# Optimization experiments

Measured on AMD Instinct MI355X. Metric: run time of the kernel, lower is better.

The kernel has to match this reference:

```python
import jax, jax.numpy as jnp
import numpy as np

# Model dims (match init_kwargs)
B, L, C = 4, 4096, 1024   # batch, seq_len, dim
M = 128                   # memory_dim
P = 4                     # n_persistent
S = 64                    # segment_size
H = 8                     # num_heads in nn.MultiheadAttention


def _ln(x, g, b, eps=1e-5):
    mu = jnp.mean(x, -1, keepdims=True)
    var = jnp.mean((x - mu) ** 2, -1, keepdims=True)
    return (x - mu) * jax.lax.rsqrt(var + eps) * g + b


def setup_inputs() -> dict:
    key = jax.random.key(0)
    ks = jax.random.split(key, 16)
    def n(k, shape, s=0.02):
        return jax.random.normal(k, shape, jnp.float32) * s
    return {
        "x": jax.random.normal(ks[0], (B, L, C), jnp.float32),
        "persistent_memory": n(ks[1], (1, P, C)),
        "Wq": n(ks[2], (C, C)),            # query_proj (no bias)
        "Wk": n(ks[3], (C, C)),            # key_proj (no bias)
        "Wv": n(ks[4], (C, C)),            # value_proj (no bias)
        # NeuralMemoryModule.memory_net: Linear(C->M), SiLU, LN(M), Linear(M->M), LN(M)
        "mem_W1": n(ks[5], (M, C)), "mem_b1": jnp.zeros((M,)),
        "mem_ln1_g": jnp.ones((M,)), "mem_ln1_b": jnp.zeros((M,)),
        "mem_W2": n(ks[6], (M, M)), "mem_b2": jnp.zeros((M,)),
        "mem_ln2_g": jnp.ones((M,)), "mem_ln2_b": jnp.zeros((M,)),
        "mem_out_W": n(ks[7], (C, M)), "mem_out_b": jnp.zeros((C,)),
        "memory_state": jnp.zeros((1, M)),  # persistent buffer (zeros at init)
        # nn.MultiheadAttention in/out projections
        "mha_Wq": n(ks[8], (C, C)), "mha_bq": jnp.zeros((C,)),
        "mha_Wk": n(ks[9], (C, C)), "mha_bk": jnp.zeros((C,)),
        "mha_Wv": n(ks[10], (C, C)), "mha_bv": jnp.zeros((C,)),
        "mha_Wo": n(ks[11], (C, C)), "mha_bo": jnp.zeros((C,)),
        "gn_g": jnp.ones((C,)), "gn_b": jnp.zeros((C,)),   # gate_norm
        "gate_W": n(ks[12], (C, C)), "gate_b": jnp.zeros((C,)),
        "out_W": n(ks[13], (C, C)), "out_b": jnp.zeros((C,)),
    }


def reference(x, persistent_memory, Wq, Wk, Wv,
              mem_W1, mem_b1, mem_ln1_g, mem_ln1_b,
              mem_W2, mem_b2, mem_ln2_g, mem_ln2_b,
              mem_out_W, mem_out_b, memory_state,
              mha_Wq, mha_bq, mha_Wk, mha_bk, mha_Wv, mha_bv, mha_Wo, mha_bo,
              gn_g, gn_b, gate_W, gate_b, out_W, out_b):
    Bx, Lx, Cx = x.shape
    n_seg = Lx // S
    # Eval-mode: memory_state is frozen, so all segments are independent ->
    # process every segment in parallel instead of a Python loop over L.
    xs = x.reshape(Bx * n_seg, S, Cx)           # [N, S, C]
    q_seg = xs @ Wq.T                            # query_proj
    # retrieve from long-term memory: memory_net(queries) + memory_state -> output_proj
    h = jax.nn.silu(q_seg @ mem_W1.T + mem_b1)
    h = _ln(h, mem_ln1_g, mem_ln1_b)
    h = h @ mem_W2.T + mem_b2
    h = _ln(h, mem_ln2_g, mem_ln2_b)             # [N, S, M]
    retrieved = (h + memory_state[0]) @ mem_out_W.T + mem_out_b  # [N, S, C]
    # context = [retrieved_memory, persistent_memory, current_segment]
    pm = jnp.broadcast_to(persistent_memory, (Bx * n_seg, P, Cx))
    context = jnp.concatenate([retrieved, pm, xs], axis=1)       # [N, T, C], T=S+P+S
    k_in = context @ Wk.T
    v_in = context @ Wv.T
    T = context.shape[1]
    hd = Cx // H
    q = (q_seg @ mha_Wq.T + mha_bq).reshape(-1, S, H, hd)
    k = (k_in @ mha_Wk.T + mha_bk).reshape(-1, T, H, hd)
    v = (v_in @ mha_Wv.T + mha_bv).reshape(-1, T, H, hd)
    scores = jnp.einsum('nshd,nthd->nhst', q, k) / jnp.sqrt(jnp.float32(hd))
    attn = jnp.einsum('nhst,nthd->nshd', jax.nn.softmax(scores, -1), v)
    attn = attn.reshape(-1, S, Cx) @ mha_Wo.T + mha_bo           # [N, S, C]
    # learned gate blend + output projection
    gate = jax.nn.sigmoid(_ln(attn, gn_g, gn_b) @ gate_W.T + gate_b)
    out = (gate * attn + xs) @ out_W.T + out_b
    return out.reshape(Bx, Lx, Cx)
```

## Files before the change

### kernel.cpp

```cpp
#include <hip/hip_runtime.h>
#include <hip/hip_bf16.h>
#include <math.h>


using bf16 = __hip_bfloat16;

typedef __attribute__((ext_vector_type(8))) short bf16x8;
typedef __attribute__((ext_vector_type(4))) float f32x4;

__device__ __forceinline__ float ldf(const bf16* p) { return __bfloat162float(*p); }
__device__ __forceinline__ float ldf(const float* p) { return *p; }
__device__ __forceinline__ void stf(bf16* p, float v) { *p = __float2bfloat16(v); }
__device__ __forceinline__ void stf(float* p, float v) { *p = v; }
__device__ __forceinline__ float b2f(const bf16& b) { return __bfloat162float(b); }
__device__ __forceinline__ float bsf(short s) {
  union { unsigned u; float f; } cv;
  cv.u = (unsigned)(unsigned short)s << 16;
  return cv.f;
}

enum { ACT_NONE = 0, ACT_SILU = 1, ACT_SIGMOID = 2, ACT_GATE = 3, ACT_PSILU = 4 };

__global__ void detect_kernel(const unsigned short* g, int* flag) {
  if (threadIdx.x == 0) *flag = (g[0] != 0) ? 1 : 0;
}

struct ConvArgs {
  const void* src[29];
  bf16* dst[29];
  int n[29];
  int bstart[30];
};

__global__ __launch_bounds__(256) void convall_kernel(ConvArgs a, const int* __restrict__ flag) {
  int b = blockIdx.x;
  int ti = 0;
  while (ti < 28 && b >= a.bstart[ti + 1]) ++ti;
  int i = (b - a.bstart[ti]) * 256 + threadIdx.x;
  if (i >= a.n[ti]) return;
  if (*flag) a.dst[ti][i] = ((const bf16*)a.src[ti])[i];
  else a.dst[ti][i] = __float2bfloat16(((const float*)a.src[ti])[i]);
}

__global__ __launch_bounds__(256) void conv_kernel(
    const void* __restrict__ src, bf16* __restrict__ dst, int n, size_t src_off,
    const int* __restrict__ flag) {
  int i = blockIdx.x * 256 + threadIdx.x;
  if (i >= n) return;
  if (*flag) dst[i] = ((const bf16*)src)[src_off + i];
  else dst[i] = __float2bfloat16(((const float*)src)[src_off + i]);
}

__global__ __launch_bounds__(256) void pack_bias4(
    const bf16* __restrict__ bk, const bf16* __restrict__ bv,
    const bf16* __restrict__ bq, const bf16* __restrict__ b1,
    bf16* __restrict__ o) {
  int j = blockIdx.x * 256 + threadIdx.x;
  if (j >= 3200) return;
  float v;
  if (j < 1024) v = b2f(bk[j]);
  else if (j < 2048) v = b2f(bv[j - 1024]);
  else if (j < 3072) v = b2f(bq[j - 2048]);
  else v = b2f(b1[j - 3072]);
  o[j] = __float2bfloat16(v);
}

__global__ __launch_bounds__(256) void transpose_kernel(
    const bf16* __restrict__ srcb, bf16* __restrict__ dstb, int rows, int cols) {
  __shared__ unsigned short t[64][72];
  const unsigned short* src = (const unsigned short*)srcb;
  unsigned short* dst = (unsigned short*)dstb;
  const int r0 = blockIdx.y * 64, c0 = blockIdx.x * 64;
  for (int e = threadIdx.x; e < 64 * 8; e += 256) {
    int r = e >> 3, c8 = e & 7;
    uint4 v = *(const uint4*)(src + (size_t)(r0 + r) * cols + c0 + c8 * 8);
    *(uint4*)&t[r][c8 * 8] = v;
  }
  __syncthreads();
  for (int e = threadIdx.x; e < 64 * 8; e += 256) {
    int c = e >> 3, r8 = (e & 7) * 8;
    unsigned short v[8];
#pragma unroll
    for (int j = 0; j < 8; ++j) v[j] = t[r8 + j][c];
    *(uint4*)(dst + (size_t)(c0 + c) * rows + r0 + r8) = *(uint4*)v;
  }
}

__global__ __launch_bounds__(256) void kpvp_kernel(
    const bf16* __restrict__ pmb, const bf16* __restrict__ mobb,
    const bf16* __restrict__ Wb, const bf16* __restrict__ bias4b,
    bf16* __restrict__ kp, bf16* __restrict__ vp, bf16* __restrict__ bkv)
{
  const short* pm = (const short*)pmb;
  const short* mob = (const short*)mobb;
  const short* W = (const short*)Wb;
  const int wave = threadIdx.x >> 6, lane = threadIdx.x & 63;
  const int c = blockIdx.x * 4 + wave;
  const short* wrow = W + (size_t)c * 1024 + lane * 16;
  const bf16x8 w0 = *(const bf16x8*)wrow;
  const bf16x8 w1 = *(const bf16x8*)(wrow + 8);
  float acc[5];
#pragma unroll
  for (int m = 0; m < 5; ++m) {
    const short* prow = (m < 4) ? (pm + m * 1024 + lane * 16) : (mob + lane * 16);
    const bf16x8 p0 = *(const bf16x8*)prow;
    const bf16x8 p1 = *(const bf16x8*)(prow + 8);
    float s = 0.f;
#pragma unroll
    for (int j = 0; j < 8; ++j) s += bsf(w0[j]) * bsf(p0[j]) + bsf(w1[j]) * bsf(p1[j]);
    acc[m] = s;
  }
#pragma unroll
  for (int d = 1; d < 64; d <<= 1) {
#pragma unroll
    for (int m = 0; m < 5; ++m) acc[m] += __shfl_xor(acc[m], d);
  }
  if (lane == 0) {
    const float bv = b2f(bias4b[c]);
    bf16* dst = (c < 1024) ? (kp + c) : (vp + (c - 1024));
#pragma unroll
    for (int m = 0; m < 4; ++m) stf(dst + m * 1024, acc[m] + bv);
    stf(&bkv[c], acc[4] + bv);
  }
}

__device__ __forceinline__ void gl_lds16(const short* g, short* l) {
  __builtin_amdgcn_global_load_lds(
      (const __attribute__((address_space(1))) void*)g,
      (__attribute__((address_space(3))) void*)l, 16, 0, 0);
}

template <typename TC, int ACT, bool HAS_BIAS>
__global__ __launch_bounds__(256) void mgemm(
    const bf16* __restrict__ Ab, const bf16* __restrict__ Bw,
    const bf16* __restrict__ bias, TC* __restrict__ C,
    int M, int N, int K, int lda, int ldc,
    const bf16* __restrict__ ao, const void* __restrict__ xsrc, size_t xoff,
    const int* __restrict__ flag, int pn)
{
  __shared__ short As[128 * 32];
  __shared__ short Bs[128 * 32];
  const short* A = (const short*)Ab;
  const short* B = (const short*)Bw;
  const int tid = threadIdx.x;
  const int m0 = blockIdx.x * 128, n0 = blockIdx.y * 128;
  const int wave = tid >> 6, lane = tid & 63;
  const int wm = (wave & 1) * 64, wn = (wave >> 1) * 64;
  const int fm = lane & 15;
  const int fk = (lane >> 4) * 8;

  const int srow = tid >> 2, scol = (tid & 3) * 8;
  const short* gA0 = A + (size_t)(m0 + srow) * lda + scol;
  const short* gA1 = A + (size_t)(m0 + 64 + srow) * lda + scol;
  const short* gB0 = B + (size_t)(n0 + srow) * K + scol;
  const short* gB1 = B + (size_t)(n0 + 64 + srow) * K + scol;
  short* lA0 = As + tid * 8;
  short* lA1 = As + (256 + tid) * 8;
  short* lB0 = Bs + tid * 8;
  short* lB1 = Bs + (256 + tid) * 8;

  f32x4 acc[4][4] = {};

  for (int k0 = 0; k0 < K; k0 += 32) {
    gl_lds16(gA0 + k0, lA0);
    gl_lds16(gA1 + k0, lA1);
    gl_lds16(gB0 + k0, lB0);
    gl_lds16(gB1 + k0, lB1);
    __syncthreads();
    bf16x8 af[4], bfr[4];
#pragma unroll
    for (int i = 0; i < 4; ++i)
      af[i] = *(const bf16x8*)&As[(wm + i * 16 + fm) * 32 + fk];
#pragma unroll
    for (int j = 0; j < 4; ++j)
      bfr[j] = *(const bf16x8*)&Bs[(wn + j * 16 + fm) * 32 + fk];
#pragma unroll
    for (int i = 0; i < 4; ++i)
#pragma unroll
      for (int j = 0; j < 4; ++j)
        acc[i][j] = __builtin_amdgcn_mfma_f32_16x16x32_bf16(af[i], bfr[j], acc[i][j], 0, 0, 0);
    __syncthreads();
  }

  const int rg = (lane >> 4) * 4;
#pragma unroll
  for (int i = 0; i < 4; ++i) {
#pragma unroll
    for (int j = 0; j < 4; ++j) {
      const int n = n0 + wn + j * 16 + fm;
      float bv = 0.f;
      if (HAS_BIAS) bv = b2f(bias[n]);
#pragma unroll
      for (int r = 0; r < 4; ++r) {
        const int m = m0 + wm + i * 16 + rg + r;
        float v = acc[i][j][r] + bv;
        if (ACT == ACT_SILU) v = v / (1.f + __expf(-v));
        if (ACT == ACT_PSILU) { if (n >= pn) v = v / (1.f + __expf(-v)); }
        if (ACT == ACT_SIGMOID) v = 1.f / (1.f + __expf(-v));
        if (ACT == ACT_GATE) {
          v = 1.f / (1.f + __expf(-v));
          const size_t e = (size_t)m * 1024 + n;
          const float xv = *flag ? b2f(((const bf16*)xsrc)[xoff + e])
                                 : ((const float*)xsrc)[xoff + e];
          v = v * b2f(ao[e]) + xv;
        }
        stf(&C[(size_t)m * ldc + n], v);
      }
    }
  }
}

__global__ __launch_bounds__(256) void kgemm(
    const bf16* __restrict__ Ab, const bf16* __restrict__ Bw,
    float* __restrict__ P, int M, int N, int K, int lda)
{
  __shared__ short As[128 * 32];
  __shared__ short Bs[128 * 32];
  const short* A = (const short*)Ab;
  const short* B = (const short*)Bw;
  const int tid = threadIdx.x;
  const int m0 = blockIdx.x * 128, n0 = blockIdx.y * 128;
  const int kb = blockIdx.z * (K >> 2), ke = kb + (K >> 2);
  const int wave = tid >> 6, lane = tid & 63;
  const int wm = (wave & 1) * 64, wn = (wave >> 1) * 64;
  const int fm = lane & 15;
  const int fk = (lane >> 4) * 8;

  const int srow = tid >> 2, scol = (tid & 3) * 8;
  const short* gA0 = A + (size_t)(m0 + srow) * lda + scol;
  const short* gA1 = A + (size_t)(m0 + 64 + srow) * lda + scol;
  const short* gB0 = B + (size_t)(n0 + srow) * K + scol;
  const short* gB1 = B + (size_t)(n0 + 64 + srow) * K + scol;
  short* lA0 = As + tid * 8;
  short* lA1 = As + (256 + tid) * 8;
  short* lB0 = Bs + tid * 8;
  short* lB1 = Bs + (256 + tid) * 8;

  f32x4 acc[4][4] = {};

  for (int k0 = kb; k0 < ke; k0 += 32) {
    gl_lds16(gA0 + k0, lA0);
    gl_lds16(gA1 + k0, lA1);
    gl_lds16(gB0 + k0, lB0);
    gl_lds16(gB1 + k0, lB1);
    __syncthreads();
    bf16x8 af[4], bfr[4];
#pragma unroll
    for (int i = 0; i < 4; ++i)
      af[i] = *(const bf16x8*)&As[(wm + i * 16 + fm) * 32 + fk];
#pragma unroll
    for (int j = 0; j < 4; ++j)
      bfr[j] = *(const bf16x8*)&Bs[(wn + j * 16 + fm) * 32 + fk];
#pragma unroll
    for (int i = 0; i < 4; ++i)
#pragma unroll
      for (int j = 0; j < 4; ++j)
        acc[i][j] = __builtin_amdgcn_mfma_f32_16x16x32_bf16(af[i], bfr[j], acc[i][j], 0, 0, 0);
    __syncthreads();
  }

  float* Cp = P + (size_t)blockIdx.z * ((size_t)M * N);
  const int rg = (lane >> 4) * 4;
#pragma unroll
  for (int i = 0; i < 4; ++i)
#pragma unroll
    for (int j = 0; j < 4; ++j) {
      const int n = n0 + wn + j * 16 + fm;
#pragma unroll
      for (int r = 0; r < 4; ++r) {
        const int m = m0 + wm + i * 16 + rg + r;
        Cp[(size_t)m * N + n] = acc[i][j][r];
      }
    }
}

__global__ __launch_bounds__(256) void foldfin_kernel(
    const float* __restrict__ P, bf16* __restrict__ o, int MN) {
  int i = blockIdx.x * 256 + threadIdx.x;
  if (i >= MN) return;
  float s = P[i] + P[i + (size_t)MN] + P[i + 2 * (size_t)MN] + P[i + 3 * (size_t)MN];
  o[i] = __float2bfloat16(s);
}

template <typename TI, typename TO, bool ADD, int W, int BS>
__global__ __launch_bounds__(BS) void ln_kernel(
    const TI* __restrict__ in, const bf16* __restrict__ g, const bf16* __restrict__ b,
    const bf16* __restrict__ addv, TO* __restrict__ out, int ldin)
{
  __shared__ float red[BS];
  const int row = blockIdx.x;
  const TI* rin = in + (size_t)row * ldin;
  TO* rout = out + (size_t)row * W;
  const int NP = W / BS;
  float v[NP];
  float s = 0.f;
#pragma unroll
  for (int i = 0; i < NP; ++i) { v[i] = ldf(&rin[threadIdx.x + i * BS]); s += v[i]; }
  red[threadIdx.x] = s; __syncthreads();
  for (int o = BS / 2; o > 0; o >>= 1) {
    if (threadIdx.x < o) red[threadIdx.x] += red[threadIdx.x + o];
    __syncthreads();
  }
  const float mean = red[0] / W;
  __syncthreads();
  float sq = 0.f;
#pragma unroll
  for (int i = 0; i < NP; ++i) { float d = v[i] - mean; sq += d * d; }
  red[threadIdx.x] = sq; __syncthreads();
  for (int o = BS / 2; o > 0; o >>= 1) {
    if (threadIdx.x < o) red[threadIdx.x] += red[threadIdx.x + o];
    __syncthreads();
  }
  const float rstd = rsqrtf(red[0] / W + 1e-5f);
#pragma unroll
  for (int i = 0; i < NP; ++i) {
    int c = threadIdx.x + i * BS;
    float o_ = (v[i] - mean) * rstd * b2f(g[c]) + b2f(b[c]);
    if (ADD) o_ += b2f(addv[c]);
    stf(&rout[c], o_);
  }
}

__global__ __launch_bounds__(512) void attn_kernel(
    const bf16* __restrict__ qg, int str_q,
    const bf16* __restrict__ krv, int str_r,
    const bf16* __restrict__ kxv, int str_x, const bf16* __restrict__ kpg,
    const bf16* __restrict__ vpg, bf16* __restrict__ outg)
{
  __shared__ short qs[4 * 64 * 32];
  __shared__ short ksl[4 * 144 * 32];
  __shared__ short vt[128 * 168];
  __shared__ short pl[64 * 168];

  const int tid = threadIdx.x;
  unsigned bid = blockIdx.x;
  {
    const unsigned nwg = gridDim.x;
    const unsigned q_ = nwg >> 3, r_ = nwg & 7;
    const unsigned xcd = bid & 7, loc = bid >> 3;
    bid = (xcd < r_ ? xcd * (q_ + 1) : r_ * (q_ + 1) + (xcd - r_) * q_) + loc;
  }
  const int seg = (int)(bid >> 3), h = (int)(bid & 7);
  const unsigned short* q = (const unsigned short*)qg + (size_t)seg * 64 * str_q + h * 128;
  const unsigned short* kv_r = (const unsigned short*)krv + (size_t)seg * 64 * str_r + h * 128;
  const unsigned short* kv_x = (const unsigned short*)kxv + (size_t)seg * 64 * str_x + h * 128;
  const unsigned short* kp = (const unsigned short*)kpg;
  const unsigned short* vp = (const unsigned short*)vpg;
  const size_t obase = (size_t)seg * 64 * 1024 + h * 128;

  for (int ch = tid; ch < 64 * 16; ch += 512) {
    int row = ch >> 4, k8 = ch & 15;
    uint4 v = *(const uint4*)(q + (size_t)row * str_q + k8 * 8);
    *(uint4*)&qs[((k8 >> 2) * 64 + row) * 32 + (k8 & 3) * 8] = v;
  }
  for (int ch = tid; ch < 132 * 16; ch += 512) {
    int t = ch >> 4, k8 = ch & 15;
    const unsigned short* src;
    if (t < 64) src = kv_r + (size_t)t * str_r;
    else if (t < 68) src = kp + (size_t)(t - 64) * 1024 + h * 128;
    else src = kv_x + (size_t)(t - 68) * str_x;
    uint4 v = *(const uint4*)(src + k8 * 8);
    *(uint4*)&ksl[((k8 >> 2) * 144 + t) * 32 + (k8 & 3) * 8] = v;
  }
  __syncthreads();

  const int wave = tid >> 6, lane = tid & 63;
  const int fm = lane & 15, fq = lane >> 4;

  if (wave < 4) {
    const int s0 = wave * 16;
    f32x4 acc[10];
#pragma unroll
    for (int tt = 0; tt < 10; ++tt) acc[tt] = (f32x4){0.f, 0.f, 0.f, 0.f};
#pragma unroll
    for (int kb = 0; kb < 4; ++kb) {
      const bf16x8 a = *(const bf16x8*)&qs[(kb * 64 + s0 + fm) * 32 + fq * 8];
#pragma unroll
      for (int tt = 0; tt < 9; ++tt) {
        const bf16x8 b = *(const bf16x8*)&ksl[(kb * 144 + tt * 16 + fm) * 32 + fq * 8];
        acc[tt] = __builtin_amdgcn_mfma_f32_16x16x32_bf16(a, b, acc[tt], 0, 0, 0);
      }
    }
    const float scale = 0.08838834764831845f;
#pragma unroll
    for (int r = 0; r < 4; ++r) {
      float m = -3.0e38f;
#pragma unroll
      for (int tt = 0; tt < 9; ++tt) {
        int t = tt * 16 + fm;
        if (t < 132) m = fmaxf(m, acc[tt][r] * scale);
      }
      for (int d = 1; d < 16; d <<= 1) m = fmaxf(m, __shfl_xor(m, d));
      float e[10];
      float sum = 0.f;
#pragma unroll
      for (int tt = 0; tt < 10; ++tt) {
        int t = tt * 16 + fm;
        float ev = 0.f;
        if (t < 132) ev = __expf(acc[tt][r] * scale - m);
        e[tt] = ev; sum += ev;
      }
      for (int d = 1; d < 16; d <<= 1) sum += __shfl_xor(sum, d);
      const float inv = 1.f / sum;
      const int s = s0 + fq * 4 + r;
#pragma unroll
      for (int tt = 0; tt < 10; ++tt) {
        bf16 pv = __float2bfloat16(e[tt] * inv);
        pl[s * 168 + tt * 16 + fm] = *(const short*)&pv;
      }
    }
  } else {
    for (int ch = tid - 256; ch < 132 * 32; ch += 256) {
      int t = ch >> 5, d4 = (ch & 31) * 4;
      const unsigned short* src;
      if (t < 64) src = kv_r + 1024 + (size_t)t * str_r;
      else if (t < 68) src = vp + (size_t)(t - 64) * 1024 + h * 128;
      else src = kv_x + 1024 + (size_t)(t - 68) * str_x;
      uint2 w = *(const uint2*)(src + d4);
      vt[(d4 + 0) * 168 + t] = (short)(w.x & 0xffffu);
      vt[(d4 + 1) * 168 + t] = (short)(w.x >> 16);
      vt[(d4 + 2) * 168 + t] = (short)(w.y & 0xffffu);
      vt[(d4 + 3) * 168 + t] = (short)(w.y >> 16);
    }
    for (int ch = tid - 256; ch < 128 * 32; ch += 256) {
      int d = ch >> 5, tp = 132 + (ch & 31);
      vt[d * 168 + tp] = 0;
    }
  }
  __syncthreads();

  const int dt = wave;
  bf16x8 af[5];
#pragma unroll
  for (int kb = 0; kb < 5; ++kb)
    af[kb] = *(const bf16x8*)&vt[(dt * 16 + fm) * 168 + kb * 32 + fq * 8];
#pragma unroll
  for (int st = 0; st < 4; ++st) {
    f32x4 o = (f32x4){0.f, 0.f, 0.f, 0.f};
#pragma unroll
    for (int kb = 0; kb < 5; ++kb) {
      const bf16x8 bp = *(const bf16x8*)&pl[(st * 16 + fm) * 168 + kb * 32 + fq * 8];
      o = __builtin_amdgcn_mfma_f32_16x16x32_bf16(af[kb], bp, o, 0, 0, 0);
    }
    const int s = st * 16 + fm;
    bf16 b0 = __float2bfloat16(o[0]), b1 = __float2bfloat16(o[1]);
    bf16 b2 = __float2bfloat16(o[2]), b3 = __float2bfloat16(o[3]);
    uint2 w;
    w.x = ((unsigned)(*(unsigned short*)&b1) << 16) | (*(unsigned short*)&b0);
    w.y = ((unsigned)(*(unsigned short*)&b3) << 16) | (*(unsigned short*)&b2);
    *(uint2*)((unsigned short*)outg + obase + (size_t)s * 1024 + dt * 16 + fq * 4) = w;
  }
}

extern "C" void kernel_launch(void* const* d_in, const int* in_sizes, int n_in,
                              void* d_out, int out_size, void* d_ws, size_t ws_size,
                              hipStream_t stream)
{
  (void)n_in; (void)out_size;
  const int R = 16384, Cd = 1024;

  char* ws = (char*)d_ws;
  size_t off = 0;
  auto alloc = [&](size_t bytes) -> void* {
    void* p = ws + off;
    off += (bytes + 255) & ~(size_t)255;
    return p;
  };

  int* flag = (int*)alloc(256);
  bf16* W4    = (bf16*)alloc((size_t)3200 * Cd * sizeof(bf16));
  bf16* bias4 = (bf16*)alloc(3200 * sizeof(bf16));
  bf16* T     = (bf16*)alloc((size_t)Cd * Cd * sizeof(bf16));
  bf16* Wc    = (bf16*)alloc((size_t)2048 * 128 * sizeof(bf16));
  bf16* kp    = (bf16*)alloc((size_t)4 * Cd * sizeof(bf16));
  bf16* vp    = (bf16*)alloc((size_t)4 * Cd * sizeof(bf16));
  bf16* bkv   = (bf16*)alloc(2048 * sizeof(bf16));
  bf16* WqStk = (bf16*)alloc((size_t)1152 * Cd * sizeof(bf16));
  bf16* nb[30];
  nb[0] = nullptr;
  for (int i = 1; i < 30; ++i) nb[i] = (bf16*)alloc((size_t)in_sizes[i] * sizeof(bf16));
  nb[16] = WqStk;
  nb[5]  = WqStk + (size_t)1024 * Cd;
  const size_t fixed_end = off;

  size_t avail = (ws_size > fixed_end + (1u << 20)) ? (ws_size - fixed_end - (1u << 20)) : 0;
  int crmax = (int)(avail / 17152);
  if (crmax > R) crmax = R;
  if (crmax < 128) crmax = 128;
  int nch = (R + crmax - 1) / crmax;
  int CR = ((R / nch + 127) / 128) * 128;
  while (CR * nch < R) CR += 128;

  const size_t chunk_start = off;
  const size_t RB = (size_t)CR * Cd * sizeof(bf16);
  bf16* Xc  = (bf16*)alloc(RB);
  bf16* QS4 = (bf16*)alloc((size_t)CR * 3200 * sizeof(bf16));
  bf16* h1b = (bf16*)alloc((size_t)CR * 128 * sizeof(bf16));
  bf16* h2b = (bf16*)alloc((size_t)CR * 128 * sizeof(bf16));
  bf16* Bb  = (bf16*)alloc(RB);
  bf16* KVr = (bf16*)alloc(2 * RB);
  bf16* Cc  = (bf16*)alloc(RB);
  const size_t chunk_bytes = off - chunk_start;

  dim3 blk(256);
  auto g128 = [](int M_, int N_) { return dim3((unsigned)(M_ / 128), (unsigned)(N_ / 128)); };

  detect_kernel<<<1, 64, 0, stream>>>((const unsigned short*)d_in[24], flag);
  {
    ConvArgs a;
    int bs = 0;
    for (int i = 1; i < 30; ++i) {
      a.src[i - 1] = d_in[i];
      a.dst[i - 1] = nb[i];
      a.n[i - 1] = in_sizes[i];
      a.bstart[i - 1] = bs;
      bs += (in_sizes[i] + 255) / 256;
    }
    a.bstart[29] = bs;
    convall_kernel<<<dim3((unsigned)bs), blk, 0, stream>>>(a, flag);
  }
  const bf16 *pm = nb[1], *Wq = nb[2], *Wk = nb[3], *Wv = nb[4];
  const bf16 *mem_W1 = nb[5], *mem_b1 = nb[6], *ln1g = nb[7], *ln1b = nb[8];
  const bf16 *mem_W2 = nb[9], *mem_b2 = nb[10], *ln2g = nb[11], *ln2b = nb[12];
  const bf16 *mem_oW = nb[13], *mem_ob = nb[14], *mstate = nb[15];
  const bf16 *mhaWq = nb[16], *mhabq = nb[17], *mhaWk = nb[18], *mhabk = nb[19];
  const bf16 *mhaWv = nb[20], *mhabv = nb[21], *mhaWo = nb[22], *mhabo = nb[23];
  const bf16 *gn_g = nb[24], *gn_b = nb[25], *gateW = nb[26], *gateb = nb[27];
  const bf16 *outW = nb[28], *outb = nb[29];
  bf16* Wkk = W4;
  bf16* Wvv = W4 + (size_t)1024 * Cd;
  bf16* Wqq = W4 + (size_t)2048 * Cd;
  bf16* Wm1 = W4 + (size_t)3072 * Cd;

  const bool use_ks = chunk_bytes >= (size_t)4 * 1152 * 1024 * sizeof(float);
  if (use_ks) {
    float* P = (float*)Xc;
    transpose_kernel<<<dim3(16, 16), blk, 0, stream>>>(Wq, T, 1024, 1024);
    kgemm<<<dim3(9, 8, 4), blk, 0, stream>>>(WqStk, T, P, 1152, 1024, 1024, 1024);
    foldfin_kernel<<<dim3(4608), blk, 0, stream>>>(P, Wqq, 1152 * 1024);
    transpose_kernel<<<dim3(16, 16), blk, 0, stream>>>(Wk, T, 1024, 1024);
    kgemm<<<dim3(8, 8, 4), blk, 0, stream>>>(mhaWk, T, P, 1024, 1024, 1024, 1024);
    foldfin_kernel<<<dim3(4096), blk, 0, stream>>>(P, Wkk, 1024 * 1024);
    transpose_kernel<<<dim3(16, 16), blk, 0, stream>>>(Wv, T, 1024, 1024);
    kgemm<<<dim3(8, 8, 4), blk, 0, stream>>>(mhaWv, T, P, 1024, 1024, 1024, 1024);
    foldfin_kernel<<<dim3(4096), blk, 0, stream>>>(P, Wvv, 1024 * 1024);
    transpose_kernel<<<dim3(2, 16), blk, 0, stream>>>(mem_oW, T, 1024, 128);
    kgemm<<<dim3(16, 1, 4), blk, 0, stream>>>(W4, T, P, 2048, 128, 1024, 1024);
    foldfin_kernel<<<dim3(1024), blk, 0, stream>>>(P, Wc, 2048 * 128);
  } else {
    transpose_kernel<<<dim3(16, 16), blk, 0, stream>>>(Wq, T, 1024, 1024);
    mgemm<bf16, ACT_NONE, false><<<g128(1024, 1024), blk, 0, stream>>>(
        mhaWq, T, nullptr, Wqq, 1024, 1024, 1024, 1024, 1024, nullptr, nullptr, 0, nullptr, 0);
    mgemm<bf16, ACT_NONE, false><<<g128(128, 1024), blk, 0, stream>>>(
        mem_W1, T, nullptr, Wm1, 128, 1024, 1024, 1024, 1024, nullptr, nullptr, 0, nullptr, 0);
    transpose_kernel<<<dim3(16, 16), blk, 0, stream>>>(Wk, T, 1024, 1024);
    mgemm<bf16, ACT_NONE, false><<<g128(1024, 1024), blk, 0, stream>>>(
        mhaWk, T, nullptr, Wkk, 1024, 1024, 1024, 1024, 1024, nullptr, nullptr, 0, nullptr, 0);
    transpose_kernel<<<dim3(16, 16), blk, 0, stream>>>(Wv, T, 1024, 1024);
    mgemm<bf16, ACT_NONE, false><<<g128(1024, 1024), blk, 0, stream>>>(
        mhaWv, T, nullptr, Wvv, 1024, 1024, 1024, 1024, 1024, nullptr, nullptr, 0, nullptr, 0);
    transpose_kernel<<<dim3(2, 16), blk, 0, stream>>>(mem_oW, T, 1024, 128);
    mgemm<bf16, ACT_NONE, false><<<g128(2048, 128), blk, 0, stream>>>(
        W4, T, nullptr, Wc, 2048, 128, 1024, 1024, 128, nullptr, nullptr, 0, nullptr, 0);
  }
  pack_bias4<<<13, blk, 0, stream>>>(mhabk, mhabv, mhabq, mem_b1, bias4);
  kpvp_kernel<<<dim3(512), blk, 0, stream>>>(pm, mem_ob, W4, bias4, kp, vp, bkv);

  for (int r0 = 0; r0 < R; r0 += CR) {
    const int cr = (R - r0 < CR) ? (R - r0) : CR;
    const int n = cr * Cd;
    conv_kernel<<<dim3((n + 255) / 256), blk, 0, stream>>>(d_in[0], Xc, n, (size_t)r0 * Cd, flag);

    mgemm<bf16, ACT_PSILU, true><<<g128(cr, 3200), blk, 0, stream>>>(
        Xc, W4, bias4, QS4, cr, 3200, 1024, 1024, 3200, nullptr, nullptr, 0, nullptr, 3072);

    ln_kernel<bf16, bf16, false, 128, 128><<<cr, 128, 0, stream>>>(
        QS4 + 3072, ln1g, ln1b, nullptr, h2b, 3200);
    mgemm<bf16, ACT_NONE, true><<<g128(cr, 128), blk, 0, stream>>>(
        h2b, mem_W2, mem_b2, h1b, cr, 128, 128, 128, 128, nullptr, nullptr, 0, nullptr, 0);
    ln_kernel<bf16, bf16, true, 128, 128><<<cr, 128, 0, stream>>>(h1b, ln2g, ln2b, mstate, h2b, 128);
    mgemm<bf16, ACT_NONE, true><<<g128(cr, 2048), blk, 0, stream>>>(
        h2b, Wc, bkv, KVr, cr, 2048, 128, 128, 2048, nullptr, nullptr, 0, nullptr, 0);

    attn_kernel<<<dim3((cr / 64) * 8), dim3(512), 0, stream>>>(
        QS4 + 2048, 3200, KVr, 2048, QS4, 3200, kp, vp, Xc);

    mgemm<bf16, ACT_NONE, true><<<g128(cr, Cd), blk, 0, stream>>>(
        Xc, mhaWo, mhabo, Bb, cr, Cd, Cd, Cd, Cd, nullptr, nullptr, 0, nullptr, 0);
    ln_kernel<bf16, bf16, false, 1024, 256><<<cr, 256, 0, stream>>>(Bb, gn_g, gn_b, nullptr, Cc, Cd);
    mgemm<bf16, ACT_GATE, true><<<g128(cr, Cd), blk, 0, stream>>>(
        Cc, gateW, gateb, Xc, cr, Cd, Cd, Cd, Cd, Bb, d_in[0], (size_t)r0 * Cd, flag, 0);
    mgemm<float, ACT_NONE, true><<<g128(cr, Cd), blk, 0, stream>>>(
        Xc, outW, outb, (float*)d_out + (size_t)r0 * Cd, cr, Cd, Cd, Cd, Cd,
        nullptr, nullptr, 0, nullptr, 0);
  }
}
```

Baseline: 884.1 us.

## Double-buffer GEMM LDS tiles with XOR swizzle and vectorize input conversion

The mgemm main loop now keeps two LDS buffers and issues the global-to-LDS loads for tile k+2 while tile k is being multiplied. Raw s_waitcnt and s_barrier calls replace the full __syncthreads pairs, so load latency can overlap with MFMA work. An XOR swizzle on the k-chunk index is applied both when writing LDS and when reading fragments, to reduce bank conflicts. The conv kernel now handles 8 elements per thread with 16-byte loads and stores. The costs are twice the LDS per block, which may lower occupancy, and the loop assumes K is at least 64 and n is a multiple of 8.

```diff
diff --git a/kernel.cpp b/kernel.cpp
--- a/kernel.cpp
+++ b/kernel.cpp
@@ -45,10 +45,21 @@
 __global__ __launch_bounds__(256) void conv_kernel(
     const void* __restrict__ src, bf16* __restrict__ dst, int n, size_t src_off,
     const int* __restrict__ flag) {
-  int i = blockIdx.x * 256 + threadIdx.x;
+  int i = (blockIdx.x * 256 + threadIdx.x) * 8;
   if (i >= n) return;
-  if (*flag) dst[i] = ((const bf16*)src)[src_off + i];
-  else dst[i] = __float2bfloat16(((const float*)src)[src_off + i]);
+  if (*flag) {
+    *(uint4*)((unsigned short*)dst + i) =
+        *(const uint4*)((const unsigned short*)src + src_off + i);
+  } else {
+    const float* s = (const float*)src + src_off + i;
+    const float4 a = *(const float4*)s;
+    const float4 b = *(const float4*)(s + 4);
+    bf16 t[8] = {__float2bfloat16(a.x), __float2bfloat16(a.y),
+                 __float2bfloat16(a.z), __float2bfloat16(a.w),
+                 __float2bfloat16(b.x), __float2bfloat16(b.y),
+                 __float2bfloat16(b.z), __float2bfloat16(b.w)};
+    *(uint4*)((unsigned short*)dst + i) = *(const uint4*)t;
+  }
 }
 
 __global__ __launch_bounds__(256) void pack_bias4(
@@ -138,8 +149,8 @@
     const bf16* __restrict__ ao, const void* __restrict__ xsrc, size_t xoff,
     const int* __restrict__ flag, int pn)
 {
-  __shared__ short As[128 * 32];
-  __shared__ short Bs[128 * 32];
+  __shared__ short As[2][128 * 32];
+  __shared__ short Bs[2][128 * 32];
   const short* A = (const short*)Ab;
   const short* B = (const short*)Bw;
   const int tid = threadIdx.x;
@@ -147,42 +158,54 @@
   const int wave = tid >> 6, lane = tid & 63;
   const int wm = (wave & 1) * 64, wn = (wave >> 1) * 64;
   const int fm = lane & 15;
-  const int fk = (lane >> 4) * 8;
-
-  const int srow = tid >> 2, scol = (tid & 3) * 8;
+  const int fq = lane >> 4;
+  const int fks = (fq ^ ((fm >> 1) & 3)) * 8;
+
+  const int srow = tid >> 2;
+  const int scol = ((tid & 3) ^ ((tid >> 3) & 3)) * 8;
   const short* gA0 = A + (size_t)(m0 + srow) * lda + scol;
   const short* gA1 = A + (size_t)(m0 + 64 + srow) * lda + scol;
   const short* gB0 = B + (size_t)(n0 + srow) * K + scol;
   const short* gB1 = B + (size_t)(n0 + 64 + srow) * K + scol;
-  short* lA0 = As + tid * 8;
-  short* lA1 = As + (256 + tid) * 8;
-  short* lB0 = Bs + tid * 8;
-  short* lB1 = Bs + (256 + tid) * 8;
 
   f32x4 acc[4][4] = {};
-
-  for (int k0 = 0; k0 < K; k0 += 32) {
-    gl_lds16(gA0 + k0, lA0);
-    gl_lds16(gA1 + k0, lA1);
-    gl_lds16(gB0 + k0, lB0);
-    gl_lds16(gB1 + k0, lB1);
-    __syncthreads();
+  const int NT = K >> 5;
+
+#define STAGE(buf, k0)                              \
+  do {                                              \
+    gl_lds16(gA0 + (k0), &As[buf][tid * 8]);        \
+    gl_lds16(gA1 + (k0), &As[buf][(256 + tid) * 8]);\
+    gl_lds16(gB0 + (k0), &Bs[buf][tid * 8]);        \
+    gl_lds16(gB1 + (k0), &Bs[buf][(256 + tid) * 8]);\
+  } while (0)
+
+  STAGE(0, 0);
+  STAGE(1, 32);
+
+  for (int kt = 0; kt < NT; ++kt) {
+    const int cur = kt & 1;
+    if (kt == NT - 1) asm volatile("s_waitcnt vmcnt(0)" ::: "memory");
+    else              asm volatile("s_waitcnt vmcnt(4)" ::: "memory");
+    __builtin_amdgcn_s_barrier();
     bf16x8 af[4], bfr[4];
 #pragma unroll
     for (int i = 0; i < 4; ++i)
-      af[i] = *(const bf16x8*)&As[(wm + i * 16 + fm) * 32 + fk];
+      af[i] = *(const bf16x8*)&As[cur][(wm + i * 16 + fm) * 32 + fks];
 #pragma unroll
     for (int j = 0; j < 4; ++j)
-      bfr[j] = *(const bf16x8*)&Bs[(wn + j * 16 + fm) * 32 + fk];
+      bfr[j] = *(const bf16x8*)&Bs[cur][(wn + j * 16 + fm) * 32 + fks];
 #pragma unroll
     for (int i = 0; i < 4; ++i)
 #pragma unroll
       for (int j = 0; j < 4; ++j)
         acc[i][j] = __builtin_amdgcn_mfma_f32_16x16x32_bf16(af[i], bfr[j], acc[i][j], 0, 0, 0);
-    __syncthreads();
-  }
-
-  const int rg = (lane >> 4) * 4;
+    asm volatile("s_waitcnt lgkmcnt(0)" ::: "memory");
+    __builtin_amdgcn_s_barrier();
+    if (kt + 2 < NT) STAGE(cur, (kt + 2) * 32);
+  }
+#undef STAGE
+
+  const int rg = fq * 4;
 #pragma unroll
   for (int i = 0; i < 4; ++i) {
 #pragma unroll
@@ -569,7 +592,8 @@
   for (int r0 = 0; r0 < R; r0 += CR) {
     const int cr = (R - r0 < CR) ? (R - r0) : CR;
     const int n = cr * Cd;
-    conv_kernel<<<dim3((n + 255) / 256), blk, 0, stream>>>(d_in[0], Xc, n, (size_t)r0 * Cd, flag);
+    conv_kernel<<<dim3((n / 8 + 255) / 256), blk, 0, stream>>>(
+        d_in[0], Xc, n, (size_t)r0 * Cd, flag);
 
     mgemm<bf16, ACT_PSILU, true><<<g128(cr, 3200), blk, 0, stream>>>(
         Xc, W4, bias4, QS4, cr, 3200, 1024, 1024, 3200, nullptr, nullptr, 0, nullptr, 3072);
```

Measured after the change: 878.7 us. Within noise of the previous version (-0.6%).
